# Kernel tuning notes

Hardware: AMD Instinct MI355X
Metric: run time of the kernel (lower is better)

Reference implementation:

```python
import jax, jax.numpy as jnp
import numpy as np

NUM_HEADS = 32
HEAD_DIM = 128
LORA_RANK = 512
Q_LORA_RANK = 1536
BSZ = 16
SEQ_LEN = 4096


def setup_inputs() -> dict:
    key = jax.random.key(0)
    k1, k2, k3, k4, k5, k6 = jax.random.split(key, 6)
    hd = NUM_HEADS * HEAD_DIM
    return {
        "hidden_states_q": jax.random.normal(k1, (BSZ, Q_LORA_RANK), dtype=jnp.float32),
        "compressed_kv": jax.random.normal(k2, (BSZ, SEQ_LEN, LORA_RANK), dtype=jnp.float32),
        # nn.Linear params: weight [out, in], bias [out]
        "Wq": jax.random.normal(k3, (hd, Q_LORA_RANK), dtype=jnp.float32) / np.sqrt(Q_LORA_RANK),
        "bq": jax.random.normal(k4, (hd,), dtype=jnp.float32) * 0.01,
        "Wkv": jax.random.normal(k5, (hd, LORA_RANK), dtype=jnp.float32) / np.sqrt(LORA_RANK),
        "bkv": jax.random.normal(k6, (hd,), dtype=jnp.float32) * 0.01,
    }


def reference(hidden_states_q, compressed_kv, Wq, bq, Wkv, bkv):
    bsz = hidden_states_q.shape[0]
    seq_len = compressed_kv.shape[1]
    # q: [b, h, d]
    q = (hidden_states_q @ Wq.T + bq).reshape(bsz, NUM_HEADS, HEAD_DIM)
    # kv decompression: [b, s, h, d] (same tensor used for both K and V)
    kv = (compressed_kv @ Wkv.T + bkv).reshape(bsz, seq_len, NUM_HEADS, HEAD_DIM)
    # attention scores per head over seq (note: original has NO 1/sqrt(d) scaling)
    attn = jnp.einsum('bhd,bshd->bhs', q, kv)
    attn = jax.nn.softmax(attn, axis=-1)
    out = jnp.einsum('bhs,bshd->bhd', attn, kv)
    return out.reshape(bsz, NUM_HEADS * HEAD_DIM)
```

## Files before the change

kernel.cpp:

```cpp
#include <hip/hip_runtime.h>

#define B  16
#define S  4096
#define R  512
#define QR 1536
#define H  32
#define D  128
#define HD 4096
#define SC 128
#define CH 32
#define KT 32
#define NT1 16

using f32x4 = __attribute__((ext_vector_type(4))) float;
using s16x8 = __attribute__((ext_vector_type(8))) short;
union bfu { s16x8 v; uint u[4]; };

typedef const void __attribute__((address_space(1)))* gas_t;
typedef void __attribute__((address_space(3)))* las_t;

__device__ __forceinline__ void gload16(const void* g, void* l) {
  __builtin_amdgcn_global_load_lds((gas_t)g, (las_t)l, 16, 0, 0);
}
__device__ __forceinline__ ushort bf_hi(float x) {
  return (ushort)(__float_as_uint(x) >> 16);
}
__device__ __forceinline__ float hi_f(float x) {
  return __uint_as_float(__float_as_uint(x) & 0xFFFF0000u);
}
__device__ __forceinline__ uint pack_hi2(float x, float y) {
  return (__float_as_uint(x) >> 16) | (__float_as_uint(y) & 0xFFFF0000u);
}
__device__ __forceinline__ ushort f2bf_rne(float x) {
  uint u = __float_as_uint(x);
  return (ushort)((u + 0x7FFFu + ((u >> 16) & 1u)) >> 16);
}
__device__ __forceinline__ float bf2f(ushort u) {
  return __uint_as_float((uint)u << 16);
}

__global__ __launch_bounds__(512) void k_q(const float* __restrict__ hsq,
                                           const float* __restrict__ Wq,
                                           const float* __restrict__ bq,
                                           float* __restrict__ q) {
  __shared__ float hs[B * QR];
  int tid = threadIdx.x;
  for (int idx = tid * 4; idx < B * QR; idx += 2048)
    *(float4*)&hs[idx] = *(const float4*)&hsq[idx];
  __syncthreads();

  int wave = tid >> 6, lane = tid & 63;
  int o = blockIdx.x * 16 + wave * 2;

  float acc0[B], acc1[B];
#pragma unroll
  for (int b = 0; b < B; ++b) { acc0[b] = 0.f; acc1[b] = 0.f; }

  const float* w0r = Wq + (size_t)o * QR;
  const float* w1r = w0r + QR;
  for (int k = lane * 4; k < QR; k += 256) {
    float4 wa = *(const float4*)&w0r[k];
    float4 wb = *(const float4*)&w1r[k];
#pragma unroll
    for (int b = 0; b < B; ++b) {
      float4 h4 = *(const float4*)&hs[b * QR + k];
      acc0[b] += wa.x * h4.x + wa.y * h4.y + wa.z * h4.z + wa.w * h4.w;
      acc1[b] += wb.x * h4.x + wb.y * h4.y + wb.z * h4.z + wb.w * h4.w;
    }
  }
#pragma unroll
  for (int b = 0; b < B; ++b) {
    float v0 = acc0[b], v1 = acc1[b];
#pragma unroll
    for (int off = 32; off > 0; off >>= 1) {
      v0 += __shfl_xor(v0, off);
      v1 += __shfl_xor(v1, off);
    }
    if (lane == 0) {
      q[b * HD + o]     = v0 + bq[o];
      q[b * HD + o + 1] = v1 + bq[o + 1];
    }
  }
}

__global__ __launch_bounds__(256) void k_qhat(const float* __restrict__ q,
                                              const float* __restrict__ Wkv,
                                              ushort* __restrict__ qhi,
                                              ushort* __restrict__ qlo) {
  int h = blockIdx.x;
  int r0 = blockIdx.y * 64;
  __shared__ float qs[B][D];
  int tid = threadIdx.x;
  for (int idx = tid; idx < B * D; idx += 256) {
    int b = idx >> 7, d = idx & (D - 1);
    qs[b][d] = q[b * HD + h * D + d];
  }
  __syncthreads();

  int r_l = tid & 63, bg = tid >> 6;
  float acc[4] = {0.f, 0.f, 0.f, 0.f};
  const float* wbase = Wkv + (size_t)(h * D) * R + r0 + r_l;
  for (int d = 0; d < D; d += 4) {
    float w0 = wbase[(d + 0) * R];
    float w1 = wbase[(d + 1) * R];
    float w2 = wbase[(d + 2) * R];
    float w3 = wbase[(d + 3) * R];
#pragma unroll
    for (int i = 0; i < 4; ++i) {
      float4 q4 = *(const float4*)&qs[bg * 4 + i][d];
      acc[i] += q4.x * w0 + q4.y * w1 + q4.z * w2 + q4.w * w3;
    }
  }
#pragma unroll
  for (int i = 0; i < 4; ++i) {
    size_t idx = ((size_t)(bg * 4 + i) * H + h) * R + r0 + r_l;
    qhi[idx] = bf_hi(acc[i]);
    qlo[idx] = bf_hi(acc[i] - hi_f(acc[i]));
  }
}

__global__ __launch_bounds__(512, 4) void k_fmha(const ushort* __restrict__ qhi,
                                                 const ushort* __restrict__ qlo,
                                                 const float* __restrict__ ckv,
                                                 ushort* __restrict__ part,
                                                 float* __restrict__ mbuf,
                                                 float* __restrict__ lbuf) {
  __shared__ __align__(16) float  csA[3][4096];
  __shared__ __align__(16) ushort qs[3][2048];
  __shared__ __align__(16) ushort Ps[H * 128];
  __shared__ float red[512];

  const int b = blockIdx.x, chunk = blockIdx.y;
  const int tid = threadIdx.x;
  const int lane = tid & 63, wv = tid >> 6;
  const int lcol = lane & 15, lgrp = lane >> 4;

  const float* cbase = ckv + ((size_t)b * S + (size_t)chunk * SC) * R;
  const ushort* qh_b = qhi + (size_t)b * H * R;
  const ushort* ql_b = qlo + (size_t)b * H * R;

  f32x4 acc[2];
  acc[0] = {0.f, 0.f, 0.f, 0.f};
  acc[1] = {0.f, 0.f, 0.f, 0.f};

  auto STAGE1 = [&](int bufsel, int kt) {
#pragma unroll
    for (int i = 0; i < 2; ++i) {
      int u = tid + 512 * i;
      int s = u >> 3;
      int jb = u & 7;
      int sb = jb ^ (s & 7);
      gload16(cbase + (size_t)s * R + kt + 4 * sb, &csA[bufsel][u * 4]);
    }
    if (tid < 256) {
      int h = tid >> 3;
      int jb = tid & 7;
      int lg = jb ^ (h & 7);
      const ushort* src = (lg < 4 ? qh_b : ql_b) + (size_t)h * R + kt + 8 * (lg & 3);
      gload16(src, &qs[bufsel][tid * 8]);
    }
  };

  auto COMPUTE1 = [&](int bufsel) {
    const int srow = 16 * wv + lcol;
    const int bkey = srow & 7;
    const float* brow = &csA[bufsel][srow * 32];
    float4 fa = *(const float4*)&brow[4 * ((2 * lgrp) ^ bkey)];
    float4 fb = *(const float4*)&brow[4 * ((2 * lgrp + 1) ^ bkey)];
    bfu bh, bl;
    bh.u[0] = pack_hi2(fa.x, fa.y); bh.u[1] = pack_hi2(fa.z, fa.w);
    bh.u[2] = pack_hi2(fb.x, fb.y); bh.u[3] = pack_hi2(fb.z, fb.w);
    bl.u[0] = pack_hi2(fa.x - hi_f(fa.x), fa.y - hi_f(fa.y));
    bl.u[1] = pack_hi2(fa.z - hi_f(fa.z), fa.w - hi_f(fa.w));
    bl.u[2] = pack_hi2(fb.x - hi_f(fb.x), fb.y - hi_f(fb.y));
    bl.u[3] = pack_hi2(fb.z - hi_f(fb.z), fb.w - hi_f(fb.w));
#pragma unroll
    for (int mt = 0; mt < 2; ++mt) {
      const int h = 16 * mt + lcol;
      const int hkey = h & 7;
      const ushort* qrow = &qs[bufsel][h * 64];
      s16x8 ah = *(const s16x8*)&qrow[8 * (lgrp ^ hkey)];
      s16x8 al = *(const s16x8*)&qrow[8 * ((4 + lgrp) ^ hkey)];
      acc[mt] = __builtin_amdgcn_mfma_f32_16x16x32_bf16(ah, bh.v, acc[mt], 0, 0, 0);
      acc[mt] = __builtin_amdgcn_mfma_f32_16x16x32_bf16(ah, bl.v, acc[mt], 0, 0, 0);
      acc[mt] = __builtin_amdgcn_mfma_f32_16x16x32_bf16(al, bh.v, acc[mt], 0, 0, 0);
    }
  };

  STAGE1(0, 0);
  STAGE1(1, KT);
#pragma unroll
  for (int t = 0; t < NT1; ++t) {
    if (t < NT1 - 1) {
      asm volatile("s_waitcnt vmcnt(2)" ::: "memory");
    } else {
      asm volatile("s_waitcnt vmcnt(0)" ::: "memory");
    }
    __builtin_amdgcn_sched_barrier(0);
    __builtin_amdgcn_s_barrier();
    COMPUTE1(t % 3);
    if (t + 2 < NT1) STAGE1((t + 2) % 3, (t + 2) * KT);
  }

  float pm[2][4];
#pragma unroll
  for (int mt = 0; mt < 2; ++mt)
#pragma unroll
    for (int i = 0; i < 4; ++i) pm[mt][i] = acc[mt][i];
#pragma unroll
  for (int off = 1; off <= 8; off <<= 1)
#pragma unroll
    for (int mt = 0; mt < 2; ++mt)
#pragma unroll
      for (int i = 0; i < 4; ++i)
        pm[mt][i] = fmaxf(pm[mt][i], __shfl_xor(pm[mt][i], off));
  if (lcol == 0) {
#pragma unroll
    for (int mt = 0; mt < 2; ++mt)
#pragma unroll
      for (int i = 0; i < 4; ++i)
        red[(16 * mt + 4 * lgrp + i) * 8 + wv] = pm[mt][i];
  }
  __syncthreads();

  float e_[2][4], psum[2][4];
#pragma unroll
  for (int mt = 0; mt < 2; ++mt)
#pragma unroll
    for (int i = 0; i < 4; ++i) {
      int h = 16 * mt + 4 * lgrp + i;
      float4 r0 = *(float4*)&red[h * 8];
      float4 r1 = *(float4*)&red[h * 8 + 4];
      float m = fmaxf(fmaxf(fmaxf(r0.x, r0.y), fmaxf(r0.z, r0.w)),
                      fmaxf(fmaxf(r1.x, r1.y), fmaxf(r1.z, r1.w)));
      float e = __expf(acc[mt][i] - m);
      e_[mt][i] = e;
      psum[mt][i] = e;
    }
#pragma unroll
  for (int off = 1; off <= 8; off <<= 1)
#pragma unroll
    for (int mt = 0; mt < 2; ++mt)
#pragma unroll
      for (int i = 0; i < 4; ++i)
        psum[mt][i] += __shfl_xor(psum[mt][i], off);
  if (lcol == 0) {
#pragma unroll
    for (int mt = 0; mt < 2; ++mt)
#pragma unroll
      for (int i = 0; i < 4; ++i)
        red[256 + (16 * mt + 4 * lgrp + i) * 8 + wv] = psum[mt][i];
  }
#pragma unroll
  for (int mt = 0; mt < 2; ++mt)
#pragma unroll
    for (int i = 0; i < 4; ++i) {
      int h = 16 * mt + 4 * lgrp + i;
      int s = 16 * wv + lcol;
      Ps[h * 128 + (((s >> 3) ^ (h & 7)) << 3) + (s & 7)] = f2bf_rne(e_[mt][i]);
    }
  __syncthreads();

  if (wv == 0 && lcol == 0) {
#pragma unroll
    for (int mt = 0; mt < 2; ++mt)
#pragma unroll
      for (int i = 0; i < 4; ++i) {
        int h = 16 * mt + 4 * lgrp + i;
        float4 r0 = *(float4*)&red[h * 8];
        float4 r1 = *(float4*)&red[h * 8 + 4];
        float M = fmaxf(fmaxf(fmaxf(r0.x, r0.y), fmaxf(r0.z, r0.w)),
                        fmaxf(fmaxf(r1.x, r1.y), fmaxf(r1.z, r1.w)));
        float4 l0 = *(float4*)&red[256 + h * 8];
        float4 l1 = *(float4*)&red[256 + h * 8 + 4];
        float L = (l0.x + l0.y + l0.z + l0.w) + (l1.x + l1.y + l1.z + l1.w);
        mbuf[((size_t)b * CH + chunk) * H + h] = M;
        lbuf[((size_t)b * CH + chunk) * H + h] = L;
      }
  }

  const int nt = wv & 1, mtr = wv >> 1;
  s16x8 bp[4];
#pragma unroll
  for (int k4 = 0; k4 < 4; ++k4) {
    int h = 16 * nt + lcol;
    int kb = 4 * k4 + lgrp;
    bp[k4] = *(const s16x8*)&Ps[h * 128 + ((kb ^ (h & 7)) << 3)];
  }

  ushort* cs2 = (ushort*)&csA[0][0];
  const int sblk = tid >> 5;
  const int rr = tid & 31;
  float fA[8], fB[8];
  ushort* pb2 = part + (size_t)(b * CH + chunk) * H * R;

  auto LOAD2 = [&](int rt) {
    const float* base = cbase + (size_t)(8 * sblk) * R + rt * 64 + rr;
#pragma unroll
    for (int j = 0; j < 8; ++j) {
      fA[j] = base[(size_t)j * R];
      fB[j] = base[(size_t)j * R + 32];
    }
  };
  auto WRITE2 = [&](int bufsel) {
    ushort* t2 = cs2 + bufsel * 8192;
    uint4 pa, pbv;
    pa.x = pack_hi2(fA[0], fA[1]); pa.y = pack_hi2(fA[2], fA[3]);
    pa.z = pack_hi2(fA[4], fA[5]); pa.w = pack_hi2(fA[6], fA[7]);
    pbv.x = pack_hi2(fB[0], fB[1]); pbv.y = pack_hi2(fB[2], fB[3]);
    pbv.z = pack_hi2(fB[4], fB[5]); pbv.w = pack_hi2(fB[6], fB[7]);
    *(uint4*)&t2[(size_t)rr * 128 + 8 * (sblk ^ (rr & 7))] = pa;
    *(uint4*)&t2[(size_t)(rr + 32) * 128 + 8 * (sblk ^ ((rr + 32) & 7))] = pbv;
  };
  auto COMPUTE2 = [&](int bufsel, int rt) {
    const ushort* t2 = cs2 + bufsel * 8192;
    const int rl = 16 * mtr + lcol;
    const int rk = rl & 7;
    f32x4 a2 = {0.f, 0.f, 0.f, 0.f};
#pragma unroll
    for (int k4 = 0; k4 < 4; ++k4) {
      s16x8 av = *(const s16x8*)&t2[(size_t)rl * 128 + 8 * ((4 * k4 + lgrp) ^ rk)];
      a2 = __builtin_amdgcn_mfma_f32_16x16x32_bf16(av, bp[k4], a2, 0, 0, 0);
    }
    uint2 w2;
    w2.x = pack_hi2(a2[0], a2[1]);
    w2.y = pack_hi2(a2[2], a2[3]);
    const int rg = rt * 64 + 16 * mtr + 4 * lgrp;
    *(uint2*)&pb2[(size_t)(16 * nt + lcol) * R + rg] = w2;
  };

  LOAD2(0);
  WRITE2(0);
  __syncthreads();
#pragma unroll
  for (int rt = 0; rt < 8; ++rt) {
    if (rt < 7) LOAD2(rt + 1);
    COMPUTE2(rt & 1, rt);
    if (rt < 7) WRITE2((rt + 1) & 1);
    __syncthreads();
  }
}

__global__ __launch_bounds__(256) void k_combine(const ushort* __restrict__ part,
                                                 const float* __restrict__ mbuf,
                                                 const float* __restrict__ lbuf,
                                                 float* __restrict__ ctx) {
  const int bid = blockIdx.x;
  const int b = bid >> 5, h = bid & 31;
  const int tid = threadIdx.x;
  float mv[CH], wv[CH];
  float M = -3.0e38f;
#pragma unroll
  for (int c = 0; c < CH; ++c) {
    mv[c] = mbuf[((size_t)b * CH + c) * H + h];
    M = fmaxf(M, mv[c]);
  }
  float denom = 0.f;
#pragma unroll
  for (int c = 0; c < CH; ++c) {
    wv[c] = __expf(mv[c] - M);
    denom += wv[c] * lbuf[((size_t)b * CH + c) * H + h];
  }
  const float inv = 1.f / denom;
  float s0 = 0.f, s1 = 0.f;
#pragma unroll
  for (int c = 0; c < CH; ++c) {
    const ushort* pp = part + (((size_t)b * CH + c) * H + h) * R;
    s0 += wv[c] * bf2f(pp[tid]);
    s1 += wv[c] * bf2f(pp[tid + 256]);
  }
  ctx[((size_t)b * H + h) * R + tid] = s0 * inv;
  ctx[((size_t)b * H + h) * R + tid + 256] = s1 * inv;
}

__global__ __launch_bounds__(256) void k_out(const float* __restrict__ ctx,
                                             const float* __restrict__ Wkv,
                                             const float* __restrict__ bkv,
                                             float* __restrict__ out) {
  int h = blockIdx.x;
  int d0 = blockIdx.y * 32;
  __shared__ float cs[B][R];
  int tid = threadIdx.x;
  for (int idx = tid * 4; idx < B * R; idx += 1024) {
    int b = idx >> 9, r = idx & 511;
    *(float4*)&cs[b][r] = *(const float4*)&ctx[(size_t)(b * H + h) * R + r];
  }
  __syncthreads();

  int dg = tid & 31;
  int bg = tid >> 5;
  int d = d0 + dg;
  int b0 = bg * 2;
  float acc0 = 0.f, acc1 = 0.f;
  const float* wrow = Wkv + ((size_t)(h * D + d)) * R;
  for (int i = 0; i < R; i += 4) {
    float4 w4 = *(const float4*)&wrow[i];
    float4 ca = *(const float4*)&cs[b0][i];
    float4 cb = *(const float4*)&cs[b0 + 1][i];
    acc0 += w4.x * ca.x + w4.y * ca.y + w4.z * ca.z + w4.w * ca.w;
    acc1 += w4.x * cb.x + w4.y * cb.y + w4.z * cb.z + w4.w * cb.w;
  }
  float bv = bkv[h * D + d];
  out[(size_t)b0 * HD + h * D + d]       = acc0 + bv;
  out[(size_t)(b0 + 1) * HD + h * D + d] = acc1 + bv;
}

extern "C" void kernel_launch(void* const* d_in, const int* in_sizes, int n_in,
                              void* d_out, int out_size, void* d_ws, size_t ws_size,
                              hipStream_t stream) {
  (void)in_sizes; (void)n_in; (void)out_size; (void)ws_size;
  const float* hsq = (const float*)d_in[0];
  const float* ckv = (const float*)d_in[1];
  const float* Wq  = (const float*)d_in[2];
  const float* bq  = (const float*)d_in[3];
  const float* Wkv = (const float*)d_in[4];
  const float* bkv = (const float*)d_in[5];
  float* out = (float*)d_out;

  float* ws   = (float*)d_ws;
  float* q    = ws;
  float* ctx  = q + 65536;
  float* mbuf = ctx + 262144;
  float* lbuf = mbuf + 16384;
  ushort* qhi  = (ushort*)(lbuf + 16384);
  ushort* qlo  = qhi + 262144;
  ushort* part = qlo + 262144;

  k_q<<<256, 512, 0, stream>>>(hsq, Wq, bq, q);
  k_qhat<<<dim3(32, 8), 256, 0, stream>>>(q, Wkv, qhi, qlo);
  k_fmha<<<dim3(B, CH), 512, 0, stream>>>(qhi, qlo, ckv, part, mbuf, lbuf);
  k_combine<<<B * H, 256, 0, stream>>>(part, mbuf, lbuf, ctx);
  k_out<<<dim3(32, 4), 256, 0, stream>>>(ctx, Wkv, bkv, out);
}
```

Baseline: 91.52 us.

## Reorder stage-1 prefetch before compute, vectorize stage-2 loads and combine stores

```diff
diff --git a/kernel.cpp b/kernel.cpp
--- a/kernel.cpp
+++ b/kernel.cpp
@@ -143,7 +143,7 @@
   acc[0] = {0.f, 0.f, 0.f, 0.f};
   acc[1] = {0.f, 0.f, 0.f, 0.f};
 
-  auto STAGE1 = [&](int bufsel, int kt) {
+  auto STAGE = [&](int bufsel, int kt) {
 #pragma unroll
     for (int i = 0; i < 2; ++i) {
       int u = tid + 512 * i;
@@ -161,7 +161,7 @@
     }
   };
 
-  auto COMPUTE1 = [&](int bufsel) {
+  auto COMPUTE = [&](int bufsel) {
     const int srow = 16 * wv + lcol;
     const int bkey = srow & 7;
     const float* brow = &csA[bufsel][srow * 32];
@@ -187,19 +187,20 @@
     }
   };
 
-  STAGE1(0, 0);
-  STAGE1(1, KT);
+  STAGE(0, 0);
+  STAGE(1, KT);
 #pragma unroll
   for (int t = 0; t < NT1; ++t) {
     if (t < NT1 - 1) {
-      asm volatile("s_waitcnt vmcnt(2)" ::: "memory");
+      if (wv < 4) asm volatile("s_waitcnt vmcnt(3)" ::: "memory");
+      else        asm volatile("s_waitcnt vmcnt(2)" ::: "memory");
     } else {
       asm volatile("s_waitcnt vmcnt(0)" ::: "memory");
     }
     __builtin_amdgcn_sched_barrier(0);
     __builtin_amdgcn_s_barrier();
-    COMPUTE1(t % 3);
-    if (t + 2 < NT1) STAGE1((t + 2) % 3, (t + 2) * KT);
+    if (t + 2 < NT1) STAGE((t + 2) % 3, (t + 2) * KT);
+    COMPUTE(t % 3);
   }
 
   float pm[2][4];
@@ -289,28 +290,34 @@
   }
 
   ushort* cs2 = (ushort*)&csA[0][0];
-  const int sblk = tid >> 5;
-  const int rr = tid & 31;
-  float fA[8], fB[8];
+  const int sA = 16 * wv + 2 * (lane >> 4);
+  const int r4 = 4 * lcol;
+  float4 ve[2], vo[2];
   ushort* pb2 = part + (size_t)(b * CH + chunk) * H * R;
 
   auto LOAD2 = [&](int rt) {
-    const float* base = cbase + (size_t)(8 * sblk) * R + rt * 64 + rr;
-#pragma unroll
-    for (int j = 0; j < 8; ++j) {
-      fA[j] = base[(size_t)j * R];
-      fB[j] = base[(size_t)j * R + 32];
+    const float* basE = cbase + (size_t)sA * R + rt * 64 + r4;
+#pragma unroll
+    for (int jj = 0; jj < 2; ++jj) {
+      const float* p = basE + (size_t)(8 * jj) * R;
+      ve[jj] = *(const float4*)p;
+      vo[jj] = *(const float4*)(p + R);
     }
   };
   auto WRITE2 = [&](int bufsel) {
     ushort* t2 = cs2 + bufsel * 8192;
-    uint4 pa, pbv;
-    pa.x = pack_hi2(fA[0], fA[1]); pa.y = pack_hi2(fA[2], fA[3]);
-    pa.z = pack_hi2(fA[4], fA[5]); pa.w = pack_hi2(fA[6], fA[7]);
-    pbv.x = pack_hi2(fB[0], fB[1]); pbv.y = pack_hi2(fB[2], fB[3]);
-    pbv.z = pack_hi2(fB[4], fB[5]); pbv.w = pack_hi2(fB[6], fB[7]);
-    *(uint4*)&t2[(size_t)rr * 128 + 8 * (sblk ^ (rr & 7))] = pa;
-    *(uint4*)&t2[(size_t)(rr + 32) * 128 + 8 * (sblk ^ ((rr + 32) & 7))] = pbv;
+    const int soff = sA & 7;
+#pragma unroll
+    for (int jj = 0; jj < 2; ++jj) {
+      const int sblk = 2 * wv + jj;
+      float fe[4] = {ve[jj].x, ve[jj].y, ve[jj].z, ve[jj].w};
+      float fo[4] = {vo[jj].x, vo[jj].y, vo[jj].z, vo[jj].w};
+#pragma unroll
+      for (int i = 0; i < 4; ++i) {
+        int r = r4 + i;
+        *(uint*)&t2[r * 128 + 8 * (sblk ^ (r & 7)) + soff] = pack_hi2(fe[i], fo[i]);
+      }
+    }
   };
   auto COMPUTE2 = [&](int bufsel, int rt) {
     const ushort* t2 = cs2 + bufsel * 8192;
@@ -366,11 +373,12 @@
 #pragma unroll
   for (int c = 0; c < CH; ++c) {
     const ushort* pp = part + (((size_t)b * CH + c) * H + h) * R;
-    s0 += wv[c] * bf2f(pp[tid]);
-    s1 += wv[c] * bf2f(pp[tid + 256]);
-  }
-  ctx[((size_t)b * H + h) * R + tid] = s0 * inv;
-  ctx[((size_t)b * H + h) * R + tid + 256] = s1 * inv;
+    uint u = *(const uint*)&pp[2 * tid];
+    s0 += wv[c] * bf2f((ushort)(u & 0xFFFFu));
+    s1 += wv[c] * bf2f((ushort)(u >> 16));
+  }
+  float2 o2 = {s0 * inv, s1 * inv};
+  *(float2*)&ctx[((size_t)b * H + h) * R + 2 * tid] = o2;
 }
 
 __global__ __launch_bounds__(256) void k_out(const float* __restrict__ ctx,
```

New measurement: 92.47 us. Within noise of the previous version (+1.0%).
